# Performance work log

Measured on AMD Instinct MI355X. Metric: run time of the kernel, lower is better.

Reference implementation:

```python
import jax, jax.numpy as jnp
import numpy as np

N_NODES = 100000
N_EDGES = 800000
NODE_DIM = 64
EDGE_DIM = 64
GEO_DIM = 8
GEO_OUT = 32
COND_DIM = 512
N_GRAPHS = 64
JOIN_DIM = EDGE_DIM + GEO_OUT  # 96


def setup_inputs() -> dict:
    key = jax.random.key(0)
    ks = jax.random.split(key, 10)
    return {
        "node_feats": jax.random.normal(ks[0], (N_NODES, NODE_DIM), jnp.float32),
        "edge_index": jax.random.randint(ks[1], (2, N_EDGES), 0, N_NODES, jnp.int64),
        "e_geo": jax.random.normal(ks[2], (N_EDGES, GEO_DIM), jnp.float32),
        "cond": jax.random.normal(ks[3], (N_GRAPHS, COND_DIM), jnp.float32),
        "edge_batch_ids": jax.random.randint(ks[4], (N_EDGES,), 0, N_GRAPHS, jnp.int64),
        "Wn": jax.random.normal(ks[5], (NODE_DIM, EDGE_DIM), jnp.float32) / np.sqrt(NODE_DIM),
        "bn": jnp.zeros((EDGE_DIM,), jnp.float32),
        "Wg": jax.random.normal(ks[6], (GEO_DIM, GEO_OUT), jnp.float32) / np.sqrt(GEO_DIM),
        "bg": jnp.zeros((GEO_OUT,), jnp.float32),
        "Wc": jax.random.normal(ks[7], (COND_DIM, 2 * EDGE_DIM), jnp.float32) / np.sqrt(COND_DIM),
        "bc": jnp.zeros((2 * EDGE_DIM,), jnp.float32),
        "Wx": jax.random.normal(ks[8], (JOIN_DIM, EDGE_DIM), jnp.float32) / np.sqrt(JOIN_DIM),
    }


def reference(node_feats, edge_index, e_geo, cond, edge_batch_ids,
              Wn, bn, Wg, bg, Wc, bc, Wx):
    # n_proj: project node features  [N, node_dim] -> [N, edge_dim]
    n_proj = node_feats @ Wn + bn
    # combine_node_attr 'mul': gather to edge endpoints and multiply  [E, edge_dim]
    src = n_proj[edge_index[0]]
    dst = n_proj[edge_index[1]]
    n_join = src * dst
    # e_geo_linear: [E, geo_dim] -> [E, geo_out]
    eg = e_geo @ Wg + bg
    # join features [E, edge_dim + geo_out]
    join = jnp.concatenate([n_join, eg], axis=-1)
    # FilmFusion: cond_proj -> gamma/beta per graph, gather to edges
    gb = cond @ Wc + bc                      # [B, 2*edge_dim]
    gamma, beta = jnp.split(gb, 2, axis=-1)
    gamma = gamma + 1.0
    gamma_e = gamma[edge_batch_ids]          # [E, edge_dim]
    beta_e = beta[edge_batch_ids]
    # x_linear (bias=False), FiLM modulation, relu
    x = join @ Wx
    return jax.nn.relu(x * gamma_e + beta_e)
```

## Files before the change

### kernel.cpp

```cpp
#include <hip/hip_runtime.h>

#define N_NODES   100000
#define N_EDGES   800000
#define NODE_DIM  64
#define EDGE_DIM  64
#define GEO_DIM   8
#define GEO_OUT   32
#define COND_DIM  512
#define N_GRAPHS  64

typedef float          f32x4 __attribute__((ext_vector_type(4)));
typedef unsigned short u16x8 __attribute__((ext_vector_type(8)));
typedef _Float16       f16x8 __attribute__((ext_vector_type(8)));
typedef _Float16       f16x2 __attribute__((ext_vector_type(2)));

__device__ __forceinline__ unsigned short f2h(float f) {
    _Float16 h = (_Float16)f;
    union { _Float16 h; unsigned short u; } cv;
    cv.h = h;
    return cv.u;
}
__device__ __forceinline__ f16x2 cvt2h(float lo, float hi) {
    f16x2 r;
    r[0] = (_Float16)lo;
    r[1] = (_Float16)hi;
    return r;
}

__global__ __launch_bounds__(128) void prep_kernel(
        const float* __restrict__ cond, const float* __restrict__ Wc,
        const float* __restrict__ bc,   const float* __restrict__ Wg,
        const float* __restrict__ bg,   const float* __restrict__ Wx,
        float* __restrict__ gamma, float* __restrict__ beta2,
        unsigned short* __restrict__ Bfrag) {
    int t = threadIdx.x;
    int g = blockIdx.x;
    if (g < N_GRAPHS) {
        __shared__ float condl[COND_DIM];
        __shared__ float gbl[128];
        for (int i = t; i < COND_DIM; i += 128) condl[i] = cond[g * COND_DIM + i];
        __syncthreads();
        float acc = bc[t];
        #pragma unroll 8
        for (int k = 0; k < COND_DIM; ++k) acc += condl[k] * Wc[k * 128 + t];
        gbl[t] = acc;
        __syncthreads();
        if (t < 64) {
            float gam = gbl[t] + 1.0f;
            float bet = gbl[64 + t];
            float cv = 0.0f;
            #pragma unroll
            for (int i = 0; i < GEO_OUT; ++i) cv += bg[i] * Wx[(64 + i) * 64 + t];
            gamma[g * 64 + t] = gam;
            beta2[g * 64 + t] = bet + cv * gam;
        }
    } else {
        for (int idx = t; idx < 6144; idx += 128) {
            int j    = idx & 7;
            int lane = (idx >> 3) & 63;
            int ct   = idx >> 9;
            int c    = ct >> 2, tt = ct & 3;
            int k = c * 32 + ((lane >> 4) & 3) * 8 + j;
            int n = tt * 16 + (lane & 15);
            float val;
            if (k < 64) {
                val = Wx[k * 64 + n];
            } else if (k < 72) {
                float s = 0.f;
                #pragma unroll
                for (int i = 0; i < GEO_OUT; ++i)
                    s += Wg[(k - 64) * GEO_OUT + i] * Wx[(64 + i) * 64 + n];
                val = s;
            } else {
                val = 0.f;
            }
            Bfrag[idx] = f2h(val);
        }
    }
}

__global__ __launch_bounds__(256) void nproj_kernel(
        const float* __restrict__ nf, const float* __restrict__ Wn,
        const float* __restrict__ bn, unsigned short* __restrict__ nprojh) {
    int lane = threadIdx.x & 63;
    int wid    = (blockIdx.x * blockDim.x + threadIdx.x) >> 6;
    int nwaves = (gridDim.x * blockDim.x) >> 6;
    float wcol[64];
    #pragma unroll
    for (int k = 0; k < 64; ++k) wcol[k] = Wn[k * 64 + lane];
    float bnl = bn[lane];
    for (int node = wid; node < N_NODES; node += nwaves) {
        int nu = __builtin_amdgcn_readfirstlane(node);
        const float* row = nf + (size_t)nu * 64;
        float a0 = 0.f, a1 = 0.f, a2 = 0.f, a3 = bnl;
        #pragma unroll
        for (int k = 0; k < 64; k += 4) {
            a0 = fmaf(row[k    ], wcol[k    ], a0);
            a1 = fmaf(row[k + 1], wcol[k + 1], a1);
            a2 = fmaf(row[k + 2], wcol[k + 2], a2);
            a3 = fmaf(row[k + 3], wcol[k + 3], a3);
        }
        nprojh[(size_t)nu * 64 + lane] = f2h((a0 + a1) + (a2 + a3));
    }
}

__global__ __launch_bounds__(256, 4) void edge_kernel(
        const unsigned short* __restrict__ nprojh,
        const int*   __restrict__ eidx,
        const float* __restrict__ egeo,
        const int*   __restrict__ ebatch,
        const unsigned short* __restrict__ Bfrag,
        const float* __restrict__ gamma,
        const float* __restrict__ beta2,
        float* __restrict__ out) {
    int lane = threadIdx.x & 63;
    int q  = lane >> 4;
    int mm = lane & 15;
    int wv = threadIdx.x >> 6;

    __shared__ unsigned short Bl[6144];
    __shared__ float ldsT[4][16 * 64];
    float* tileb = ldsT[wv];

    for (int i = threadIdx.x; i < 768; i += 256)
        ((f32x4*)Bl)[i] = ((const f32x4*)Bfrag)[i];
    __syncthreads();

    int wid    = (blockIdx.x * blockDim.x + threadIdx.x) >> 6;
    int nwaves = (gridDim.x * blockDim.x) >> 6;
    const int NT = N_EDGES / 16;

    int sA, dA, bqA[4];
    int bqC[4];
    u16x8 s0, s1, d0, d1;
    f32x4 g0 = {0,0,0,0}, g1 = {0,0,0,0};

    int tile = wid;
    {
        int e0 = tile * 16;
        sA = __builtin_nontemporal_load(eidx + e0 + mm);
        dA = __builtin_nontemporal_load(eidx + N_EDGES + e0 + mm);
        #pragma unroll
        for (int c = 0; c < 4; ++c)
            bqA[c] = __builtin_nontemporal_load(ebatch + e0 + c * 4 + q);
        const u16x8* ps = (const u16x8*)(nprojh + (size_t)sA * 64 + q * 8);
        const u16x8* pd = (const u16x8*)(nprojh + (size_t)dA * 64 + q * 8);
        s0 = ps[0]; s1 = ps[4];
        d0 = pd[0]; d1 = pd[4];
        if (q == 0) {
            g0 = __builtin_nontemporal_load((const f32x4*)(egeo + (size_t)(e0 + mm) * 8));
            g1 = __builtin_nontemporal_load((const f32x4*)(egeo + (size_t)(e0 + mm) * 8 + 4));
        }
        #pragma unroll
        for (int c = 0; c < 4; ++c) bqC[c] = bqA[c];
        int tn = tile + nwaves;
        if (tn < NT) {
            int e0n = tn * 16;
            sA = __builtin_nontemporal_load(eidx + e0n + mm);
            dA = __builtin_nontemporal_load(eidx + N_EDGES + e0n + mm);
            #pragma unroll
            for (int c = 0; c < 4; ++c)
                bqA[c] = __builtin_nontemporal_load(ebatch + e0n + c * 4 + q);
        }
    }

    for (; tile < NT; tile += nwaves) {
        int e0  = tile * 16;
        int tn  = tile + nwaves;
        int tnn = tn + nwaves;
        bool hasN  = tn  < NT;
        bool hasNN = tnn < NT;

        union HU { u16x8 v; f16x2 h[4]; unsigned u[4]; f16x8 f; };
        HU S0, S1, D0, D1, A0, A1, A2;
        S0.v = s0; S1.v = s1; D0.v = d0; D1.v = d1;
        #pragma unroll
        for (int j = 0; j < 4; ++j) {
            A0.h[j] = S0.h[j] * D0.h[j];
            A1.h[j] = S1.h[j] * D1.h[j];
            A2.u[j] = 0u;
        }
        if (q == 0) {
            A2.h[0] = cvt2h(g0[0], g0[1]);
            A2.h[1] = cvt2h(g0[2], g0[3]);
            A2.h[2] = cvt2h(g1[0], g1[1]);
            A2.h[3] = cvt2h(g1[2], g1[3]);
        }

        int sB, dB, bqB[4];
        if (hasNN) {
            int e0nn = tnn * 16;
            sB = __builtin_nontemporal_load(eidx + e0nn + mm);
            dB = __builtin_nontemporal_load(eidx + N_EDGES + e0nn + mm);
            #pragma unroll
            for (int c = 0; c < 4; ++c)
                bqB[c] = __builtin_nontemporal_load(ebatch + e0nn + c * 4 + q);
        }
        if (hasN) {
            const u16x8* ps = (const u16x8*)(nprojh + (size_t)sA * 64 + q * 8);
            const u16x8* pd = (const u16x8*)(nprojh + (size_t)dA * 64 + q * 8);
            s0 = ps[0]; s1 = ps[4];
            d0 = pd[0]; d1 = pd[4];
            int e0n = tn * 16;
            if (q == 0) {
                g0 = __builtin_nontemporal_load((const f32x4*)(egeo + (size_t)(e0n + mm) * 8));
                g1 = __builtin_nontemporal_load((const f32x4*)(egeo + (size_t)(e0n + mm) * 8 + 4));
            }
        }

        f32x4 acc[4];
        #pragma unroll
        for (int t = 0; t < 4; ++t) {
            f32x4 c = {0.f, 0.f, 0.f, 0.f};
            c = __builtin_amdgcn_mfma_f32_16x16x32_f16(
                    A0.f, *(const f16x8*)(Bl + (size_t)((0 * 4 + t) * 64 + lane) * 8), c, 0, 0, 0);
            c = __builtin_amdgcn_mfma_f32_16x16x32_f16(
                    A1.f, *(const f16x8*)(Bl + (size_t)((1 * 4 + t) * 64 + lane) * 8), c, 0, 0, 0);
            c = __builtin_amdgcn_mfma_f32_16x16x32_f16(
                    A2.f, *(const f16x8*)(Bl + (size_t)((2 * 4 + t) * 64 + lane) * 8), c, 0, 0, 0);
            acc[t] = c;
        }

        #pragma unroll
        for (int t = 0; t < 4; ++t)
            #pragma unroll
            for (int i = 0; i < 4; ++i)
                tileb[(q * 4 + i) * 64 + t * 16 + mm] = acc[t][i];
        asm volatile("s_waitcnt lgkmcnt(0)" ::: "memory");
        #pragma unroll
        for (int c = 0; c < 4; ++c) {
            int row = c * 4 + q;
            int b   = bqC[c];
            f32x4 v  = *(const f32x4*)&tileb[row * 64 + mm * 4];
            f32x4 gm = *(const f32x4*)(gamma + b * 64 + mm * 4);
            f32x4 bt = *(const f32x4*)(beta2 + b * 64 + mm * 4);
            f32x4 r;
            #pragma unroll
            for (int i = 0; i < 4; ++i) {
                float x = fmaf(v[i], gm[i], bt[i]);
                r[i] = x > 0.f ? x : 0.f;
            }
            __builtin_nontemporal_store(r, (f32x4*)(out + (size_t)e0 * 64 + c * 256 + lane * 4));
        }

        #pragma unroll
        for (int c = 0; c < 4; ++c) bqC[c] = bqA[c];
        if (hasNN) {
            sA = sB; dA = dB;
            #pragma unroll
            for (int c = 0; c < 4; ++c) bqA[c] = bqB[c];
        }
    }
}

extern "C" void kernel_launch(void* const* d_in, const int* in_sizes, int n_in,
                              void* d_out, int out_size, void* d_ws, size_t ws_size,
                              hipStream_t stream) {
    const float* node_feats = (const float*)d_in[0];
    const int*   edge_index = (const int*)  d_in[1];
    const float* e_geo      = (const float*)d_in[2];
    const float* cond       = (const float*)d_in[3];
    const int*   ebatch     = (const int*)  d_in[4];
    const float* Wn         = (const float*)d_in[5];
    const float* bn         = (const float*)d_in[6];
    const float* Wg         = (const float*)d_in[7];
    const float* bg         = (const float*)d_in[8];
    const float* Wc         = (const float*)d_in[9];
    const float* bc         = (const float*)d_in[10];
    const float* Wx         = (const float*)d_in[11];
    float* out = (float*)d_out;

    char* ws = (char*)d_ws;
    float*          gamma  = (float*)(ws);
    float*          beta2  = (float*)(ws + 16384);
    unsigned short* Bfrag  = (unsigned short*)(ws + 32768);
    unsigned short* nprojh = (unsigned short*)(ws + 49152);

    hipLaunchKernelGGL(prep_kernel, dim3(65), dim3(128), 0, stream,
                       cond, Wc, bc, Wg, bg, Wx, gamma, beta2, Bfrag);
    hipLaunchKernelGGL(nproj_kernel, dim3(3125), dim3(256), 0, stream,
                       node_feats, Wn, bn, nprojh);
    hipLaunchKernelGGL(edge_kernel, dim3(3125), dim3(256), 0, stream,
                       nprojh, edge_index, e_geo, ebatch, Bfrag, gamma, beta2, out);
}
```

Baseline: 369.8 us.

## Merge prep and node-projection kernels; fully unroll edge loop with double-buffered gathers

Folds the small prep kernel and the node-projection kernel into one launch, so the FiLM/weight prep blocks run alongside the node projection and one kernel boundary disappears. The edge kernel drops its generic grid-stride loop. Each wave now handles exactly four tiles through a straight-line sequence with two register sets that alternate, so gathers for tile i+2 are issued while tile i computes. This hardcodes the edge count to exactly 4 tiles per wave for this grid size and raises register pressure.

```diff
diff --git a/kernel.cpp b/kernel.cpp
--- a/kernel.cpp
+++ b/kernel.cpp
@@ -9,6 +9,10 @@
 #define COND_DIM  512
 #define N_GRAPHS  64
 
+#define PREP_BLOCKS   65
+#define NPROJ_BLOCKS  3125
+#define EDGE_BLOCKS   3125
+
 typedef float          f32x4 __attribute__((ext_vector_type(4)));
 typedef unsigned short u16x8 __attribute__((ext_vector_type(8)));
 typedef _Float16       f16x8 __attribute__((ext_vector_type(8)));
@@ -27,23 +31,27 @@
     return r;
 }
 
-__global__ __launch_bounds__(128) void prep_kernel(
+__global__ __launch_bounds__(256) void pre_kernel(
         const float* __restrict__ cond, const float* __restrict__ Wc,
         const float* __restrict__ bc,   const float* __restrict__ Wg,
         const float* __restrict__ bg,   const float* __restrict__ Wx,
+        const float* __restrict__ nf,   const float* __restrict__ Wn,
+        const float* __restrict__ bn,
         float* __restrict__ gamma, float* __restrict__ beta2,
-        unsigned short* __restrict__ Bfrag) {
+        unsigned short* __restrict__ Bfrag, unsigned short* __restrict__ nprojh) {
     int t = threadIdx.x;
     int g = blockIdx.x;
     if (g < N_GRAPHS) {
         __shared__ float condl[COND_DIM];
         __shared__ float gbl[128];
-        for (int i = t; i < COND_DIM; i += 128) condl[i] = cond[g * COND_DIM + i];
+        for (int i = t; i < COND_DIM; i += 256) condl[i] = cond[g * COND_DIM + i];
         __syncthreads();
-        float acc = bc[t];
-        #pragma unroll 8
-        for (int k = 0; k < COND_DIM; ++k) acc += condl[k] * Wc[k * 128 + t];
-        gbl[t] = acc;
+        if (t < 128) {
+            float acc = bc[t];
+            #pragma unroll 8
+            for (int k = 0; k < COND_DIM; ++k) acc += condl[k] * Wc[k * 128 + t];
+            gbl[t] = acc;
+        }
         __syncthreads();
         if (t < 64) {
             float gam = gbl[t] + 1.0f;
@@ -54,8 +62,8 @@
             gamma[g * 64 + t] = gam;
             beta2[g * 64 + t] = bet + cv * gam;
         }
-    } else {
-        for (int idx = t; idx < 6144; idx += 128) {
+    } else if (g == N_GRAPHS) {
+        for (int idx = t; idx < 6144; idx += 256) {
             int j    = idx & 7;
             int lane = (idx >> 3) & 63;
             int ct   = idx >> 9;
@@ -76,31 +84,27 @@
             }
             Bfrag[idx] = f2h(val);
         }
-    }
-}
-
-__global__ __launch_bounds__(256) void nproj_kernel(
-        const float* __restrict__ nf, const float* __restrict__ Wn,
-        const float* __restrict__ bn, unsigned short* __restrict__ nprojh) {
-    int lane = threadIdx.x & 63;
-    int wid    = (blockIdx.x * blockDim.x + threadIdx.x) >> 6;
-    int nwaves = (gridDim.x * blockDim.x) >> 6;
-    float wcol[64];
-    #pragma unroll
-    for (int k = 0; k < 64; ++k) wcol[k] = Wn[k * 64 + lane];
-    float bnl = bn[lane];
-    for (int node = wid; node < N_NODES; node += nwaves) {
-        int nu = __builtin_amdgcn_readfirstlane(node);
-        const float* row = nf + (size_t)nu * 64;
-        float a0 = 0.f, a1 = 0.f, a2 = 0.f, a3 = bnl;
+    } else {
+        int lane = t & 63;
+        int wid    = ((g - PREP_BLOCKS) * 256 + t) >> 6;
+        const int nwaves = (NPROJ_BLOCKS * 256) >> 6;
+        float wcol[64];
         #pragma unroll
-        for (int k = 0; k < 64; k += 4) {
-            a0 = fmaf(row[k    ], wcol[k    ], a0);
-            a1 = fmaf(row[k + 1], wcol[k + 1], a1);
-            a2 = fmaf(row[k + 2], wcol[k + 2], a2);
-            a3 = fmaf(row[k + 3], wcol[k + 3], a3);
-        }
-        nprojh[(size_t)nu * 64 + lane] = f2h((a0 + a1) + (a2 + a3));
+        for (int k = 0; k < 64; ++k) wcol[k] = Wn[k * 64 + lane];
+        float bnl = bn[lane];
+        for (int node = wid; node < N_NODES; node += nwaves) {
+            int nu = __builtin_amdgcn_readfirstlane(node);
+            const float* row = nf + (size_t)nu * 64;
+            float a0 = 0.f, a1 = 0.f, a2 = 0.f, a3 = bnl;
+            #pragma unroll
+            for (int k = 0; k < 64; k += 4) {
+                a0 = fmaf(row[k    ], wcol[k    ], a0);
+                a1 = fmaf(row[k + 1], wcol[k + 1], a1);
+                a2 = fmaf(row[k + 2], wcol[k + 2], a2);
+                a3 = fmaf(row[k + 3], wcol[k + 3], a3);
+            }
+            nprojh[(size_t)nu * 64 + lane] = f2h((a0 + a1) + (a2 + a3));
+        }
     }
 }
 
@@ -126,131 +130,117 @@
         ((f32x4*)Bl)[i] = ((const f32x4*)Bfrag)[i];
     __syncthreads();
 
-    int wid    = (blockIdx.x * blockDim.x + threadIdx.x) >> 6;
-    int nwaves = (gridDim.x * blockDim.x) >> 6;
-    const int NT = N_EDGES / 16;
-
-    int sA, dA, bqA[4];
-    int bqC[4];
-    u16x8 s0, s1, d0, d1;
-    f32x4 g0 = {0,0,0,0}, g1 = {0,0,0,0};
-
-    int tile = wid;
+    int wid = (blockIdx.x * blockDim.x + threadIdx.x) >> 6;
+    const int nwaves = (EDGE_BLOCKS * 256) >> 6;
+    const int t0 = wid;
+
+    union HU { u16x8 v; f16x2 h[4]; unsigned u[4]; f16x8 f; };
+
+    HU   sA0, sA1, dA0, dA1;  f32x4 gA0 = {0,0,0,0}, gA1 = {0,0,0,0};
+    HU   sB0, sB1, dB0, dB1;  f32x4 gB0 = {0,0,0,0}, gB1 = {0,0,0,0};
+    int  bqA[4], bqB[4];
+    int  siA, diA, bqiA[4];
+    int  siB, diB, bqiB[4];
+
+#define LOAD_IDX(sI, dI, bqI, tl)                                              \
+    {                                                                          \
+        int e0n = (tl) * 16;                                                   \
+        sI = __builtin_nontemporal_load(eidx + e0n + mm);                      \
+        dI = __builtin_nontemporal_load(eidx + N_EDGES + e0n + mm);            \
+        _Pragma("unroll")                                                      \
+        for (int c = 0; c < 4; ++c)                                            \
+            bqI[c] = __builtin_nontemporal_load(ebatch + e0n + c * 4 + q);     \
+    }
+
+#define GATHER(S0, S1, D0, D1, G0, G1, sI, dI, tl)                             \
+    {                                                                          \
+        const u16x8* ps = (const u16x8*)(nprojh + (size_t)(sI) * 64 + q * 8);  \
+        const u16x8* pd = (const u16x8*)(nprojh + (size_t)(dI) * 64 + q * 8);  \
+        S0.v = ps[0]; S1.v = ps[4];                                            \
+        D0.v = pd[0]; D1.v = pd[4];                                            \
+        if (q == 0) {                                                          \
+            int e0n = (tl) * 16;                                               \
+            G0 = __builtin_nontemporal_load((const f32x4*)(egeo + (size_t)(e0n + mm) * 8));     \
+            G1 = __builtin_nontemporal_load((const f32x4*)(egeo + (size_t)(e0n + mm) * 8 + 4)); \
+        }                                                                      \
+    }
+
     {
-        int e0 = tile * 16;
-        sA = __builtin_nontemporal_load(eidx + e0 + mm);
-        dA = __builtin_nontemporal_load(eidx + N_EDGES + e0 + mm);
-        #pragma unroll
-        for (int c = 0; c < 4; ++c)
-            bqA[c] = __builtin_nontemporal_load(ebatch + e0 + c * 4 + q);
-        const u16x8* ps = (const u16x8*)(nprojh + (size_t)sA * 64 + q * 8);
-        const u16x8* pd = (const u16x8*)(nprojh + (size_t)dA * 64 + q * 8);
-        s0 = ps[0]; s1 = ps[4];
-        d0 = pd[0]; d1 = pd[4];
-        if (q == 0) {
-            g0 = __builtin_nontemporal_load((const f32x4*)(egeo + (size_t)(e0 + mm) * 8));
-            g1 = __builtin_nontemporal_load((const f32x4*)(egeo + (size_t)(e0 + mm) * 8 + 4));
-        }
-        #pragma unroll
-        for (int c = 0; c < 4; ++c) bqC[c] = bqA[c];
-        int tn = tile + nwaves;
-        if (tn < NT) {
-            int e0n = tn * 16;
-            sA = __builtin_nontemporal_load(eidx + e0n + mm);
-            dA = __builtin_nontemporal_load(eidx + N_EDGES + e0n + mm);
-            #pragma unroll
-            for (int c = 0; c < 4; ++c)
-                bqA[c] = __builtin_nontemporal_load(ebatch + e0n + c * 4 + q);
-        }
-    }
-
-    for (; tile < NT; tile += nwaves) {
-        int e0  = tile * 16;
-        int tn  = tile + nwaves;
-        int tnn = tn + nwaves;
-        bool hasN  = tn  < NT;
-        bool hasNN = tnn < NT;
-
-        union HU { u16x8 v; f16x2 h[4]; unsigned u[4]; f16x8 f; };
-        HU S0, S1, D0, D1, A0, A1, A2;
-        S0.v = s0; S1.v = s1; D0.v = d0; D1.v = d1;
-        #pragma unroll
-        for (int j = 0; j < 4; ++j) {
-            A0.h[j] = S0.h[j] * D0.h[j];
-            A1.h[j] = S1.h[j] * D1.h[j];
-            A2.u[j] = 0u;
-        }
-        if (q == 0) {
-            A2.h[0] = cvt2h(g0[0], g0[1]);
-            A2.h[1] = cvt2h(g0[2], g0[3]);
-            A2.h[2] = cvt2h(g1[0], g1[1]);
-            A2.h[3] = cvt2h(g1[2], g1[3]);
-        }
-
-        int sB, dB, bqB[4];
-        if (hasNN) {
-            int e0nn = tnn * 16;
-            sB = __builtin_nontemporal_load(eidx + e0nn + mm);
-            dB = __builtin_nontemporal_load(eidx + N_EDGES + e0nn + mm);
-            #pragma unroll
-            for (int c = 0; c < 4; ++c)
-                bqB[c] = __builtin_nontemporal_load(ebatch + e0nn + c * 4 + q);
-        }
-        if (hasN) {
-            const u16x8* ps = (const u16x8*)(nprojh + (size_t)sA * 64 + q * 8);
-            const u16x8* pd = (const u16x8*)(nprojh + (size_t)dA * 64 + q * 8);
-            s0 = ps[0]; s1 = ps[4];
-            d0 = pd[0]; d1 = pd[4];
-            int e0n = tn * 16;
-            if (q == 0) {
-                g0 = __builtin_nontemporal_load((const f32x4*)(egeo + (size_t)(e0n + mm) * 8));
-                g1 = __builtin_nontemporal_load((const f32x4*)(egeo + (size_t)(e0n + mm) * 8 + 4));
-            }
-        }
-
-        f32x4 acc[4];
-        #pragma unroll
-        for (int t = 0; t < 4; ++t) {
-            f32x4 c = {0.f, 0.f, 0.f, 0.f};
-            c = __builtin_amdgcn_mfma_f32_16x16x32_f16(
-                    A0.f, *(const f16x8*)(Bl + (size_t)((0 * 4 + t) * 64 + lane) * 8), c, 0, 0, 0);
-            c = __builtin_amdgcn_mfma_f32_16x16x32_f16(
-                    A1.f, *(const f16x8*)(Bl + (size_t)((1 * 4 + t) * 64 + lane) * 8), c, 0, 0, 0);
-            c = __builtin_amdgcn_mfma_f32_16x16x32_f16(
-                    A2.f, *(const f16x8*)(Bl + (size_t)((2 * 4 + t) * 64 + lane) * 8), c, 0, 0, 0);
-            acc[t] = c;
-        }
-
-        #pragma unroll
-        for (int t = 0; t < 4; ++t)
-            #pragma unroll
-            for (int i = 0; i < 4; ++i)
-                tileb[(q * 4 + i) * 64 + t * 16 + mm] = acc[t][i];
-        asm volatile("s_waitcnt lgkmcnt(0)" ::: "memory");
-        #pragma unroll
-        for (int c = 0; c < 4; ++c) {
-            int row = c * 4 + q;
-            int b   = bqC[c];
-            f32x4 v  = *(const f32x4*)&tileb[row * 64 + mm * 4];
-            f32x4 gm = *(const f32x4*)(gamma + b * 64 + mm * 4);
-            f32x4 bt = *(const f32x4*)(beta2 + b * 64 + mm * 4);
-            f32x4 r;
-            #pragma unroll
-            for (int i = 0; i < 4; ++i) {
-                float x = fmaf(v[i], gm[i], bt[i]);
-                r[i] = x > 0.f ? x : 0.f;
-            }
-            __builtin_nontemporal_store(r, (f32x4*)(out + (size_t)e0 * 64 + c * 256 + lane * 4));
-        }
-
-        #pragma unroll
-        for (int c = 0; c < 4; ++c) bqC[c] = bqA[c];
-        if (hasNN) {
-            sA = sB; dA = dB;
-            #pragma unroll
-            for (int c = 0; c < 4; ++c) bqA[c] = bqB[c];
-        }
-    }
+        int si, di;
+        LOAD_IDX(si, di, bqA, t0);
+        GATHER(sA0, sA1, dA0, dA1, gA0, gA1, si, di, t0);
+        LOAD_IDX(si, di, bqB, t0 + nwaves);
+        GATHER(sB0, sB1, dB0, dB1, gB0, gB1, si, di, t0 + nwaves);
+        LOAD_IDX(siA, diA, bqiA, t0 + 2 * nwaves);
+        LOAD_IDX(siB, diB, bqiB, t0 + 3 * nwaves);
+    }
+
+#define BODY(S0, S1, D0, D1, G0, G1, BQ, tl, PREF, sI, dI, bqI)                \
+    {                                                                          \
+        int e0 = (tl) * 16;                                                    \
+        HU A0, A1, A2;                                                         \
+        _Pragma("unroll")                                                      \
+        for (int j = 0; j < 4; ++j) {                                          \
+            A0.h[j] = S0.h[j] * D0.h[j];                     \
+            A1.h[j] = S1.h[j] * D1.h[j];                                       \
+            A2.u[j] = 0u;                                                      \
+        }                                                                      \
+        if (q == 0) {                         \
+            A2.h[0] = cvt2h(G0[0], G0[1]);                                     \
+            A2.h[1] = cvt2h(G0[2], G0[3]);                                     \
+            A2.h[2] = cvt2h(G1[0], G1[1]);                                     \
+            A2.h[3] = cvt2h(G1[2], G1[3]);                                     \
+        }                                                                      \
+        if (PREF)                                  \
+            GATHER(S0, S1, D0, D1, G0, G1, sI, dI, (tl) + 2 * nwaves);         \
+        f32x4 acc[4];                                                          \
+        _Pragma("unroll")                                                      \
+        for (int t = 0; t < 4; ++t) {                                          \
+            f32x4 c = {0.f, 0.f, 0.f, 0.f};                                    \
+            c = __builtin_amdgcn_mfma_f32_16x16x32_f16(                        \
+                    A0.f, *(const f16x8*)(Bl + ((0 * 4 + t) * 64 + lane) * 8), c, 0, 0, 0); \
+            c = __builtin_amdgcn_mfma_f32_16x16x32_f16(                        \
+                    A1.f, *(const f16x8*)(Bl + ((1 * 4 + t) * 64 + lane) * 8), c, 0, 0, 0); \
+            c = __builtin_amdgcn_mfma_f32_16x16x32_f16(                        \
+                    A2.f, *(const f16x8*)(Bl + ((2 * 4 + t) * 64 + lane) * 8), c, 0, 0, 0); \
+            acc[t] = c;                                                        \
+        }                                                                      \
+        _Pragma("unroll")                                                      \
+        for (int t = 0; t < 4; ++t)                                            \
+            _Pragma("unroll")                                                  \
+            for (int i = 0; i < 4; ++i)                                        \
+                tileb[(q * 4 + i) * 64 + t * 16 + mm] = acc[t][i];             \
+        asm volatile("s_waitcnt lgkmcnt(0)" ::: "memory");      \
+        _Pragma("unroll")                                                      \
+        for (int c2 = 0; c2 < 4; ++c2) {                                       \
+            int row = c2 * 4 + q;                                              \
+            int b   = BQ[c2];                                                  \
+            f32x4 v  = *(const f32x4*)&tileb[row * 64 + mm * 4];               \
+            f32x4 gm = *(const f32x4*)(gamma + b * 64 + mm * 4);               \
+            f32x4 bt = *(const f32x4*)(beta2 + b * 64 + mm * 4);               \
+            f32x4 r;                                                           \
+            _Pragma("unroll")                                                  \
+            for (int i = 0; i < 4; ++i) {                                      \
+                float x = fmaf(v[i], gm[i], bt[i]);                            \
+                r[i] = x > 0.f ? x : 0.f;                                      \
+            }                                                                  \
+            __builtin_nontemporal_store(r,                                     \
+                (f32x4*)(out + (size_t)e0 * 64 + c2 * 256 + lane * 4));        \
+        }                                                                      \
+        if (PREF) {                                                            \
+            _Pragma("unroll")                                                  \
+            for (int c2 = 0; c2 < 4; ++c2) BQ[c2] = bqI[c2];                   \
+        }                                                                      \
+    }
+
+    BODY(sA0, sA1, dA0, dA1, gA0, gA1, bqA, t0,              true,  siA, diA, bqiA);
+    BODY(sB0, sB1, dB0, dB1, gB0, gB1, bqB, t0 + nwaves,     true,  siB, diB, bqiB);
+    BODY(sA0, sA1, dA0, dA1, gA0, gA1, bqA, t0 + 2 * nwaves, false, siA, diA, bqiA);
+    BODY(sB0, sB1, dB0, dB1, gB0, gB1, bqB, t0 + 3 * nwaves, false, siB, diB, bqiB);
+
+#undef BODY
+#undef GATHER
+#undef LOAD_IDX
 }
 
 extern "C" void kernel_launch(void* const* d_in, const int* in_sizes, int n_in,
@@ -276,10 +266,9 @@
     unsigned short* Bfrag  = (unsigned short*)(ws + 32768);
     unsigned short* nprojh = (unsigned short*)(ws + 49152);
 
-    hipLaunchKernelGGL(prep_kernel, dim3(65), dim3(128), 0, stream,
-                       cond, Wc, bc, Wg, bg, Wx, gamma, beta2, Bfrag);
-    hipLaunchKernelGGL(nproj_kernel, dim3(3125), dim3(256), 0, stream,
-                       node_feats, Wn, bn, nprojh);
-    hipLaunchKernelGGL(edge_kernel, dim3(3125), dim3(256), 0, stream,
+    hipLaunchKernelGGL(pre_kernel, dim3(PREP_BLOCKS + NPROJ_BLOCKS), dim3(256), 0, stream,
+                       cond, Wc, bc, Wg, bg, Wx, node_feats, Wn, bn,
+                       gamma, beta2, Bfrag, nprojh);
+    hipLaunchKernelGGL(edge_kernel, dim3(EDGE_BLOCKS), dim3(256), 0, stream,
                        nprojh, edge_index, e_geo, ebatch, Bfrag, gamma, beta2, out);
 }
```

Measured after the change: 345.6 us. 1.07x faster.
